# Kernel optimization log

Hardware: AMD Instinct MI355X
Metric: run time of the kernel (lower is better)

Reference implementation:

```python
import jax, jax.numpy as jnp
import numpy as np

EPS = 1e-6  # NAFNet LayerNorm2d eps
C = 64
B, H, W = 4, 128, 512


def _layer_norm_c(x, w, b):
    # x: [B,H,W,C]; normalize over channel dim (LayerNorm2d semantics)
    mu = jnp.mean(x, axis=-1, keepdims=True)
    var = jnp.mean(jnp.square(x - mu), axis=-1, keepdims=True)
    return (x - mu) * jax.lax.rsqrt(var + EPS) * w + b


def setup_inputs() -> dict:
    key = jax.random.key(0)
    ks = jax.random.split(key, 8)
    std = 1.0 / np.sqrt(C)  # conv1x1 fan-in init scale
    return {
        "x_l": jax.random.normal(ks[0], (B, C, H, W), jnp.float32),
        "x_r": jax.random.normal(ks[1], (B, C, H, W), jnp.float32),
        "norm_l_w": jnp.ones((C,), jnp.float32),
        "norm_l_b": jnp.zeros((C,), jnp.float32),
        "norm_r_w": jnp.ones((C,), jnp.float32),
        "norm_r_b": jnp.zeros((C,), jnp.float32),
        "l1_w": jax.random.normal(ks[2], (C, C), jnp.float32) * std,
        "l1_b": jnp.zeros((C,), jnp.float32),
        "r1_w": jax.random.normal(ks[3], (C, C), jnp.float32) * std,
        "r1_b": jnp.zeros((C,), jnp.float32),
        "l2_w": jax.random.normal(ks[4], (C, C), jnp.float32) * std,
        "l2_b": jnp.zeros((C,), jnp.float32),
        "r2_w": jax.random.normal(ks[5], (C, C), jnp.float32) * std,
        "r2_b": jnp.zeros((C,), jnp.float32),
        "beta": jax.random.normal(ks[6], (C,), jnp.float32) * 0.1,
        "gamma": jax.random.normal(ks[7], (C,), jnp.float32) * 0.1,
    }


def reference(x_l, x_r, norm_l_w, norm_l_b, norm_r_w, norm_r_b,
              l1_w, l1_b, r1_w, r1_b, l2_w, l2_b, r2_w, r2_b, beta, gamma):
    c = x_l.shape[1]
    scale = c ** (-0.5)
    # NCHW -> NHWC for channel-last math
    xl = jnp.transpose(x_l, (0, 2, 3, 1))  # [B,H,W,C]
    xr = jnp.transpose(x_r, (0, 2, 3, 1))

    # 1x1 conv == per-pixel linear: y = x @ W^T + b (W is [out,in])
    Q_l = jnp.einsum("bhwc,oc->bhwo", _layer_norm_c(xl, norm_l_w, norm_l_b), l1_w) + l1_b
    Q_r = jnp.einsum("bhwc,oc->bhwo", _layer_norm_c(xr, norm_r_w, norm_r_b), r1_w) + r1_b
    V_l = jnp.einsum("bhwc,oc->bhwo", xl, l2_w) + l2_b
    V_r = jnp.einsum("bhwc,oc->bhwo", xr, r2_w) + r2_b

    # row-wise cross-attention scores: [B,H,W_l,W_r]
    att = jnp.einsum("bhwc,bhvc->bhwv", Q_l, Q_r) * scale

    # right->left: softmax over W_r (last axis)
    F_r2l = jnp.einsum("bhwv,bhvc->bhwc", jax.nn.softmax(att, axis=-1), V_r)
    # left->right: softmax over W_l (axis -2 of att)
    F_l2r = jnp.einsum("bhwv,bhwc->bhvc", jax.nn.softmax(att, axis=-2), V_l)

    out_l = x_l + jnp.transpose(F_r2l * beta, (0, 3, 1, 2))
    out_r = x_r + jnp.transpose(F_l2r * gamma, (0, 3, 1, 2))
    return out_l, out_r
```

## Files before the change

### kernel.cpp

```cpp
#include <hip/hip_runtime.h>
#include <hip/hip_bf16.h>

#define HW_   65536
#define CHW_  4194304
#define OUTR_ 16777216
#define QSZ_  16777216

typedef __attribute__((ext_vector_type(4))) float    f32x4;
typedef __attribute__((ext_vector_type(8))) short    s16x8;
typedef __attribute__((ext_vector_type(4))) short    s16x4;
typedef __attribute__((ext_vector_type(4))) unsigned u32x4;
typedef __attribute__((ext_vector_type(2))) unsigned u32x2;

#define MFMA32(A,B,C) __builtin_amdgcn_mfma_f32_16x16x32_bf16((A),(B),(C),0,0,0)

#if __has_builtin(__builtin_amdgcn_mfma_f32_16x16x16bf16_1k)
#define MFMA16(A,B,C) __builtin_amdgcn_mfma_f32_16x16x16bf16_1k((A),(B),(C),0,0,0)
#else
__device__ __forceinline__ f32x4 mfma16_asm(s16x4 a, s16x4 b, f32x4 c){
  asm volatile("v_mfma_f32_16x16x16_bf16 %0, %1, %2, %0\n\ts_nop 7" : "+v"(c) : "v"(a), "v"(b));
  return c;
}
#define MFMA16(A,B,C) mfma16_asm((A),(B),(C))
#endif

#if __has_builtin(__builtin_amdgcn_exp2f)
#define EXP2(x) __builtin_amdgcn_exp2f(x)
#else
__device__ __forceinline__ float exp2_hw(float x){
  float r; asm("v_exp_f32 %0, %1\n\ts_nop 0" : "=v"(r) : "v"(x)); return r;
}
#define EXP2(x) exp2_hw(x)
#endif

#define QSCALE  0.18033688011112043f
#define SQSCALE 0.42466090350f

__device__ __forceinline__ unsigned short bf16u(float f) {
  union { __hip_bfloat16 h; unsigned short s; } x; x.h = __float2bfloat16(f); return x.s;
}
__device__ __forceinline__ unsigned pack2(float a, float b) {
  return (unsigned)bf16u(a) | ((unsigned)bf16u(b) << 16);
}
__device__ __forceinline__ float bflo(unsigned u) {
  union { unsigned q; float f; } x; x.q = u << 16; return x.f;
}
__device__ __forceinline__ float bfhi(unsigned u) {
  union { unsigned q; float f; } x; x.q = u & 0xFFFF0000u; return x.f;
}
__device__ __forceinline__ s16x8 as_s16x8(u32x4 u){ union{u32x4 a; s16x8 b;} x; x.a=u; return x.b; }
__device__ __forceinline__ s16x4 as_s16x4(u32x2 u){ union{u32x2 a; s16x4 b;} x; x.a=u; return x.b; }

__device__ __forceinline__ int swz128(int row, int bir) { return row*128 + (bir ^ ((row&7)<<4)); }
__device__ __forceinline__ int swzV(int c, int bir)    { return c*1024 + (bir ^ ((c&63)<<4)); }

__device__ __forceinline__ void ln32(const float* __restrict__ p, int base, int pix, int half,
                                     const float* __restrict__ w, const float* __restrict__ bb,
                                     char* buf, float* redS, float* redSS) {
  const int c0 = half*32;
  float xv[32], s = 0.f, ss = 0.f;
#pragma unroll
  for (int i = 0; i < 32; ++i) {
    float v = p[base + (c0+i)*HW_ + pix];
    xv[i] = v; s += v; ss = fmaf(v, v, ss);
  }
  redS[half*512 + pix] = s; redSS[half*512 + pix] = ss;
  __syncthreads();
  float st  = redS[pix]  + redS[512 + pix];
  float sst = redSS[pix] + redSS[512 + pix];
  float mu = st * 0.015625f;
  float rs = rsqrtf(fmaxf(sst * 0.015625f - mu*mu, 0.f) + 1e-6f);
#pragma unroll
  for (int i2 = 0; i2 < 4; ++i2) {
    u32x4 u;
#pragma unroll
    for (int e = 0; e < 4; ++e) {
      int i = i2*8 + e*2;
      float y0 = (xv[i  ]-mu)*rs*w[c0+i  ] + bb[c0+i  ];
      float y1 = (xv[i+1]-mu)*rs*w[c0+i+1] + bb[c0+i+1];
      u[e] = pack2(y0, y1);
    }
    *(u32x4*)(buf + swz128(pix, half*64 + i2*16)) = u;
  }
}

__device__ __forceinline__ void stageW(const float* __restrict__ Wg, char* bufW, int t) {
  int row = t >> 3, c0 = (t & 7) * 8;
  f32x4 f0 = *(const f32x4*)(Wg + row*64 + c0);
  f32x4 f1 = *(const f32x4*)(Wg + row*64 + c0 + 4);
  u32x4 u = { pack2(f0[0],f0[1]), pack2(f0[2],f0[3]), pack2(f1[0],f1[1]), pack2(f1[2],f1[3]) };
  *(u32x4*)(bufW + swz128(row, c0*2)) = u;
}

__device__ __forceinline__ void epi32(const char* bufG, const float* __restrict__ xres,
                                      const float* __restrict__ coef, float* __restrict__ outp,
                                      int base, int pix, int half) {
  const int c0 = half*32;
#pragma unroll
  for (int i2 = 0; i2 < 4; ++i2) {
    u32x4 gv = *(const u32x4*)(bufG + swz128(pix, half*64 + i2*16));
#pragma unroll
    for (int e = 0; e < 4; ++e) {
      int i = i2*8 + e*2;
      int idx = base + (c0+i)*HW_ + pix;
      outp[idx]       = xres[idx]       + coef[c0+i]   * bflo(gv[e]);
      outp[idx + HW_] = xres[idx + HW_] + coef[c0+i+1] * bfhi(gv[e]);
    }
  }
}

__global__ __launch_bounds__(1024)
void k1_prep(const float* __restrict__ xl, const float* __restrict__ xr,
             const float* __restrict__ nlw, const float* __restrict__ nlb,
             const float* __restrict__ nrw, const float* __restrict__ nrb,
             const float* __restrict__ l1w, const float* __restrict__ l1b,
             const float* __restrict__ r1w, const float* __restrict__ r1b,
             unsigned short* __restrict__ Qws) {
  __shared__ __align__(16) char bufA[65536];
  __shared__ __align__(16) char bufW[8192];
  __shared__ float redS[1024], redSS[1024];
  const int t = threadIdx.x, lane = t & 63, wave = t >> 6;
  const int pix = t & 511, half = t >> 9;
  const int g = lane >> 4, q15 = lane & 15;
  const int bh = blockIdx.x, b = bh >> 7, h = bh & 127;
  const int base = b*CHW_ + h*512;

#pragma unroll 1
  for (int s = 0; s < 2; ++s) {
    const float* x  = s ? xr  : xl;
    const float* w  = s ? nrw : nlw;
    const float* bb = s ? nrb : nlb;
    const float* W  = s ? r1w : l1w;
    const float* bi = s ? r1b : l1b;
    unsigned short* Qd = Qws + s*QSZ_ + bh*32768;
    if (s) __syncthreads();
    ln32(x, base, pix, half, w, bb, bufA, redS, redSS);
    if (t < 512) stageW(W, bufW, t);
    __syncthreads();
    {
      u32x4 a[2][2], wb[4][2];
#pragma unroll
      for (int mt = 0; mt < 2; ++mt)
#pragma unroll
        for (int hh = 0; hh < 2; ++hh)
          a[mt][hh] = *(const u32x4*)(bufA + swz128(wave*32 + mt*16 + q15, hh*64 + g*16));
#pragma unroll
      for (int ot = 0; ot < 4; ++ot)
#pragma unroll
        for (int hh = 0; hh < 2; ++hh)
          wb[ot][hh] = *(const u32x4*)(bufW + swz128(ot*16 + q15, hh*64 + g*16));
#pragma unroll
      for (int mt = 0; mt < 2; ++mt)
#pragma unroll
        for (int ot = 0; ot < 4; ++ot) {
          f32x4 z = {0.f,0.f,0.f,0.f};
          f32x4 acc = MFMA32(as_s16x8(a[mt][0]), as_s16x8(wb[ot][0]), z);
          acc = MFMA32(as_s16x8(a[mt][1]), as_s16x8(wb[ot][1]), acc);
          float bv = bi[ot*16 + q15];
#pragma unroll
          for (int rr = 0; rr < 4; ++rr)
            *(short*)(bufA + swz128(wave*32 + mt*16 + 4*g + rr, 2*(ot*16 + q15))) =
                (short)bf16u((acc[rr] + bv) * SQSCALE);
        }
    }
    __syncthreads();
#pragma unroll
    for (int i = 0; i < 4; ++i) {
      int seg = t*4 + i, row = seg >> 3, b16 = (seg & 7) * 16;
      u32x4 v = *(const u32x4*)(bufA + swz128(row, b16));
      *(u32x4*)((char*)Qd + row*128 + b16) = v;
    }
  }
}

__global__ __launch_bounds__(512)
void k2_fused(const unsigned short* __restrict__ Qws,
              const float* __restrict__ xl, const float* __restrict__ xr,
              const float* __restrict__ l2w, const float* __restrict__ l2b,
              const float* __restrict__ r2w, const float* __restrict__ r2b,
              const float* __restrict__ beta, const float* __restrict__ gamma,
              float* __restrict__ out) {
  __shared__ __align__(16) char ldsM[40960];
  __shared__ float lsumS[256];
  char* const Kc0 = ldsM;
  char* const Vc0 = ldsM + 16384;
  char* const bufW = ldsM + 32768;

  const int t = threadIdx.x, lane = t & 63, wave = t >> 6;
  const int g = lane >> 4, q15 = lane & 15;
  const int bid = blockIdx.x, qh = bid & 1, dir = (bid >> 1) & 1, bh = bid >> 2;
  const int b = bh >> 7, h = bh & 127;
  const int base = b*CHW_ + h*512;
  const char* Qb = (const char*)(Qws + dir*QSZ_ + bh*32768);
  const char* Kb = (const char*)(Qws + (1-dir)*QSZ_ + bh*32768);
  const float* xV   = dir ? xl : xr;
  const float* xres = dir ? xr : xl;
  const float* W2   = dir ? l2w : r2w;
  const float* b2   = dir ? l2b : r2b;
  const float* cf   = dir ? gamma : beta;
  float* outp = out + dir*OUTR_;

  const int qrow0 = qh*256 + wave*32;
  s16x8 qf[2][2];
#pragma unroll
  for (int qt = 0; qt < 2; ++qt)
#pragma unroll
    for (int hh = 0; hh < 2; ++hh)
      qf[qt][hh] = as_s16x8(*(const u32x4*)(Qb + (qrow0 + qt*16 + q15)*128 + hh*64 + g*16));

  stageW(W2, bufW, t);

  const int srow = t >> 3, sg = (t & 7) * 16, kv0 = (t & 7) * 8;
  {
    *(u32x4*)(Kc0 + swz128(srow, sg)) = *(const u32x4*)(Kb + srow*128 + sg);
    f32x4 f0 = *(const f32x4*)(xV + base + srow*HW_ + kv0);
    f32x4 f1 = *(const f32x4*)(xV + base + srow*HW_ + kv0 + 4);
    u32x4 vv = { pack2(f0[0],f0[1]), pack2(f0[2],f0[3]), pack2(f1[0],f1[1]), pack2(f1[2],f1[3]) };
    *(u32x4*)(Vc0 + swz128(srow, sg)) = vv;
  }
  __syncthreads();

  float lsum[2] = {0.f, 0.f};
  f32x4 O[2][4];
#pragma unroll
  for (int qt = 0; qt < 2; ++qt)
#pragma unroll
    for (int ct = 0; ct < 4; ++ct) { f32x4 z = {0.f,0.f,0.f,0.f}; O[qt][ct] = z; }

#pragma unroll 1
  for (int ch = 0; ch < 8; ++ch) {
    char* const Kc = Kc0 + (ch & 1)*8192;
    char* const Vc = Vc0 + (ch & 1)*8192;
    u32x4 kreg; f32x4 nf0, nf1;
    if (ch < 7) {
      kreg = *(const u32x4*)(Kb + ((ch+1)*64 + srow)*128 + sg);
      nf0  = *(const f32x4*)(xV + base + srow*HW_ + (ch+1)*64 + kv0);
      nf1  = *(const f32x4*)(xV + base + srow*HW_ + (ch+1)*64 + kv0 + 4);
    }
#pragma unroll
    for (int qt = 0; qt < 2; ++qt) {
      u32x2 pa[4];
      float sml = 0.f;
#pragma unroll
      for (int kb = 0; kb < 4; ++kb) {
        u32x4 k0 = *(const u32x4*)(Kc + swz128(kb*16 + q15, g*16));
        u32x4 k1 = *(const u32x4*)(Kc + swz128(kb*16 + q15, 64 + g*16));
        f32x4 z = {0.f,0.f,0.f,0.f};
        f32x4 s = MFMA32(as_s16x8(k0), qf[qt][0], z);
        s = MFMA32(as_s16x8(k1), qf[qt][1], s);
        float p0 = EXP2(s[0]), p1 = EXP2(s[1]), p2 = EXP2(s[2]), p3 = EXP2(s[3]);
        sml += (p0 + p1) + (p2 + p3);
        u32x2 pp = { pack2(p0, p1), pack2(p2, p3) };
        pa[kb] = pp;
      }
      lsum[qt] += sml;
#pragma unroll
      for (int ct = 0; ct < 4; ++ct) {
        int c = ct*16 + q15;
#pragma unroll
        for (int kb = 0; kb < 4; ++kb) {
          u32x2 vb = *(const u32x2*)(Vc + swz128(c, kb*32 + 8*g));
          O[qt][ct] = MFMA16(as_s16x4(pa[kb]), as_s16x4(vb), O[qt][ct]);
        }
      }
    }
    if (ch < 7) {
      char* const Kn = Kc0 + ((ch & 1)^1)*8192;
      char* const Vn = Vc0 + ((ch & 1)^1)*8192;
      *(u32x4*)(Kn + swz128(srow, sg)) = kreg;
      u32x4 vv = { pack2(nf0[0],nf0[1]), pack2(nf0[2],nf0[3]), pack2(nf1[0],nf1[1]), pack2(nf1[2],nf1[3]) };
      *(u32x4*)(Vn + swz128(srow, sg)) = vv;
    }
    __syncthreads();
  }

#pragma unroll
  for (int qt = 0; qt < 2; ++qt) {
    float l = lsum[qt];
    l += __shfl_xor(l, 16);
    l += __shfl_xor(l, 32);
    if (lane < 16) lsumS[wave*32 + qt*16 + q15] = l;
#pragma unroll
    for (int ct = 0; ct < 4; ++ct)
#pragma unroll
      for (int rr = 0; rr < 4; ++rr)
        *(short*)(ldsM + swz128(wave*32 + qt*16 + 4*g + rr, 2*(ct*16 + q15))) =
            (short)bf16u(O[qt][ct][rr]);
  }
  __syncthreads();

  {
    u32x4 a[2][2], wb[4][2];
#pragma unroll
    for (int mt = 0; mt < 2; ++mt)
#pragma unroll
      for (int hh = 0; hh < 2; ++hh)
        a[mt][hh] = *(const u32x4*)(ldsM + swz128(wave*32 + mt*16 + q15, hh*64 + g*16));
#pragma unroll
    for (int ot = 0; ot < 4; ++ot)
#pragma unroll
      for (int hh = 0; hh < 2; ++hh)
        wb[ot][hh] = *(const u32x4*)(bufW + swz128(ot*16 + q15, hh*64 + g*16));
#pragma unroll
    for (int mt = 0; mt < 2; ++mt)
#pragma unroll
      for (int ot = 0; ot < 4; ++ot) {
        f32x4 z = {0.f,0.f,0.f,0.f};
        f32x4 acc = MFMA32(as_s16x8(a[mt][0]), as_s16x8(wb[ot][0]), z);
        acc = MFMA32(as_s16x8(a[mt][1]), as_s16x8(wb[ot][1]), acc);
#pragma unroll
        for (int rr = 0; rr < 4; ++rr)
          *(short*)(ldsM + swz128(wave*32 + mt*16 + 4*g + rr, 2*(ot*16 + q15))) =
              (short)bf16u(acc[rr]);
      }
  }
  __syncthreads();

  {
    const int pl = t & 255, half2 = t >> 8;
    const int pix = qh*256 + pl;
    const float il = 1.f / lsumS[pl];
    const int c0 = half2*32;
#pragma unroll
    for (int i2 = 0; i2 < 4; ++i2) {
      u32x4 gv = *(const u32x4*)(ldsM + swz128(pl, half2*64 + i2*16));
#pragma unroll
      for (int e = 0; e < 4; ++e) {
        int c = c0 + i2*8 + e*2;
        int idx = base + c*HW_ + pix;
        outp[idx]       = xres[idx]       + cf[c]  *(bflo(gv[e])*il + b2[c]);
        outp[idx + HW_] = xres[idx + HW_] + cf[c+1]*(bfhi(gv[e])*il + b2[c+1]);
      }
    }
  }
}

__device__ __forceinline__ void stageV_m(const float* __restrict__ x, int base, char* bufV, int t) {
  int c = t >> 4, w0 = (t & 15) * 32;
#pragma unroll
  for (int i = 0; i < 4; ++i) {
    int w = w0 + i*8;
    f32x4 f0 = *(const f32x4*)(x + base + c*HW_ + w);
    f32x4 f1 = *(const f32x4*)(x + base + c*HW_ + w + 4);
    u32x4 u = { pack2(f0[0],f0[1]), pack2(f0[2],f0[3]), pack2(f1[0],f1[1]), pack2(f1[2],f1[3]) };
    *(u32x4*)(bufV + swzV(c, w*2)) = u;
  }
}
__device__ __forceinline__ void proj64_m(const char* bufIn, const char* bufW,
                                         const float* __restrict__ biasG,
                                         char* bufOut, int wave, int lane) {
  int g = lane >> 4, q15 = lane & 15;
  u32x4 a[2][2], wb[4][2];
#pragma unroll
  for (int mt = 0; mt < 2; ++mt)
#pragma unroll
    for (int h = 0; h < 2; ++h)
      a[mt][h] = *(const u32x4*)(bufIn + swz128(wave*32 + mt*16 + q15, h*64 + g*16));
#pragma unroll
  for (int ot = 0; ot < 4; ++ot)
#pragma unroll
    for (int h = 0; h < 2; ++h)
      wb[ot][h] = *(const u32x4*)(bufW + swz128(ot*16 + q15, h*64 + g*16));
#pragma unroll
  for (int mt = 0; mt < 2; ++mt)
#pragma unroll
    for (int ot = 0; ot < 4; ++ot) {
      f32x4 z = {0.f,0.f,0.f,0.f};
      f32x4 acc = MFMA32(as_s16x8(a[mt][0]), as_s16x8(wb[ot][0]), z);
      acc = MFMA32(as_s16x8(a[mt][1]), as_s16x8(wb[ot][1]), acc);
      float bv = biasG[ot*16 + q15];
#pragma unroll
      for (int rr = 0; rr < 4; ++rr)
        *(short*)(bufOut + swz128(wave*32 + mt*16 + 4*g + rr, 2*(ot*16 + q15))) =
            (short)bf16u(acc[rr] + bv);
    }
}
__device__ __forceinline__ void extract_q_m(const char* bufQ, int wave, int lane, s16x8 (&qf)[2][2]) {
  int g = lane >> 4, q15 = lane & 15;
#pragma unroll
  for (int qt = 0; qt < 2; ++qt)
#pragma unroll
    for (int h = 0; h < 2; ++h) {
      u32x4 u = *(const u32x4*)(bufQ + swz128(wave*32 + qt*16 + q15, h*64 + g*16));
#pragma unroll
      for (int e = 0; e < 4; ++e)
        u[e] = pack2(bflo(u[e])*QSCALE, bfhi(u[e])*QSCALE);
      qf[qt][h] = as_s16x8(u);
    }
}
__device__ __forceinline__ void flash_m(const char* bufK, const char* bufV, const s16x8 (&qf)[2][2],
                                        f32x4 (&O)[2][4], float (&lsum)[2], int lane) {
  int g = lane >> 4, q15 = lane & 15;
  float mref[2];
#pragma unroll
  for (int qt = 0; qt < 2; ++qt) {
    mref[qt] = -__builtin_inff(); lsum[qt] = 0.f;
#pragma unroll
    for (int ct = 0; ct < 4; ++ct) { f32x4 z = {0.f,0.f,0.f,0.f}; O[qt][ct] = z; }
  }
#pragma unroll 1
  for (int ch = 0; ch < 16; ++ch) {
    int kbase = ch * 32;
    u32x4 ka[2][2];
#pragma unroll
    for (int kb = 0; kb < 2; ++kb)
#pragma unroll
      for (int h = 0; h < 2; ++h)
        ka[kb][h] = *(const u32x4*)(bufK + swz128(kbase + kb*16 + q15, h*64 + g*16));
#pragma unroll
    for (int qt = 0; qt < 2; ++qt) {
      f32x4 z = {0.f,0.f,0.f,0.f};
      f32x4 a0 = MFMA32(as_s16x8(ka[0][0]), qf[qt][0], z);
      a0 = MFMA32(as_s16x8(ka[0][1]), qf[qt][1], a0);
      f32x4 a1 = MFMA32(as_s16x8(ka[1][0]), qf[qt][0], z);
      a1 = MFMA32(as_s16x8(ka[1][1]), qf[qt][1], a1);
      float cm = fmaxf(fmaxf(fmaxf(a0[0],a0[1]), fmaxf(a0[2],a0[3])),
                       fmaxf(fmaxf(a1[0],a1[1]), fmaxf(a1[2],a1[3])));
      cm = fmaxf(cm, __shfl_xor(cm, 16));
      cm = fmaxf(cm, __shfl_xor(cm, 32));
      if (__any(cm > mref[qt] + 8.f)) {
        float nm = fmaxf(mref[qt], cm);
        float corr = EXP2(mref[qt] - nm);
        lsum[qt] *= corr; mref[qt] = nm;
#pragma unroll
        for (int rr = 0; rr < 4; ++rr) {
          float cr = __shfl(corr, 4*g + rr);
#pragma unroll
          for (int ct = 0; ct < 4; ++ct) O[qt][ct][rr] *= cr;
        }
      }
      float p[8], sm = 0.f;
#pragma unroll
      for (int j = 0; j < 4; ++j) { p[j]   = EXP2(a0[j] - mref[qt]); sm += p[j]; }
#pragma unroll
      for (int j = 0; j < 4; ++j) { p[4+j] = EXP2(a1[j] - mref[qt]); sm += p[4+j]; }
      float s1 = sm + __shfl_xor(sm, 16);
      lsum[qt] += s1 + __shfl_xor(s1, 32);
      u32x2 pa0 = { pack2(p[0],p[1]), pack2(p[2],p[3]) };
      u32x2 pa1 = { pack2(p[4],p[5]), pack2(p[6],p[7]) };
#pragma unroll
      for (int ct = 0; ct < 4; ++ct) {
        int c = ct*16 + q15;
        u32x2 v0 = *(const u32x2*)(bufV + swzV(c, (kbase + 4*g)*2));
        u32x2 v1 = *(const u32x2*)(bufV + swzV(c, (kbase + 16 + 4*g)*2));
        O[qt][ct] = MFMA16(as_s16x4(pa0), as_s16x4(v0), O[qt][ct]);
        O[qt][ct] = MFMA16(as_s16x4(pa1), as_s16x4(v1), O[qt][ct]);
      }
    }
  }
}
__device__ __forceinline__ void write_O_m(char* buf, const f32x4 (&O)[2][4], const float (&lsum)[2],
                                          int wave, int lane) {
  int g = lane >> 4, q15 = lane & 15;
#pragma unroll
  for (int qt = 0; qt < 2; ++qt) {
    float inv = 1.f / lsum[qt];
    float invr[4];
#pragma unroll
    for (int rr = 0; rr < 4; ++rr) invr[rr] = __shfl(inv, 4*g + rr);
#pragma unroll
    for (int ct = 0; ct < 4; ++ct)
#pragma unroll
      for (int rr = 0; rr < 4; ++rr)
        *(short*)(buf + swz128(wave*32 + qt*16 + 4*g + rr, 2*(ct*16 + q15))) =
            (short)bf16u(O[qt][ct][rr] * invr[rr]);
  }
}
__device__ __forceinline__ void epi_ln_m(const char* bufG, const float* __restrict__ xres,
                                         const float* __restrict__ coef, float* __restrict__ outp,
                                         const float* __restrict__ w, const float* __restrict__ bb,
                                         char* bufLN, int base, int pix, int half,
                                         float* redS, float* redSS) {
  const int c0 = half*32;
  float xv[32], s = 0.f, ss = 0.f;
#pragma unroll
  for (int i2 = 0; i2 < 4; ++i2) {
    u32x4 gv = *(const u32x4*)(bufG + swz128(pix, half*64 + i2*16));
#pragma unroll
    for (int e = 0; e < 4; ++e) {
      int i = i2*8 + e*2;
      int idx = base + (c0+i)*HW_ + pix;
      float x0 = xres[idx], x1 = xres[idx + HW_];
      xv[i] = x0; xv[i+1] = x1;
      s += x0 + x1; ss = fmaf(x0,x0,ss); ss = fmaf(x1,x1,ss);
      outp[idx]       = x0 + coef[c0+i]   * bflo(gv[e]);
      outp[idx + HW_] = x1 + coef[c0+i+1] * bfhi(gv[e]);
    }
  }
  redS[half*512 + pix] = s; redSS[half*512 + pix] = ss;
  __syncthreads();
  float st  = redS[pix]  + redS[512 + pix];
  float sst = redSS[pix] + redSS[512 + pix];
  float mu = st * 0.015625f;
  float rs = rsqrtf(fmaxf(sst * 0.015625f - mu*mu, 0.f) + 1e-6f);
#pragma unroll
  for (int i2 = 0; i2 < 4; ++i2) {
    u32x4 u;
#pragma unroll
    for (int e = 0; e < 4; ++e) {
      int i = i2*8 + e*2;
      float y0 = (xv[i  ]-mu)*rs*w[c0+i  ] + bb[c0+i  ];
      float y1 = (xv[i+1]-mu)*rs*w[c0+i+1] + bb[c0+i+1];
      u[e] = pack2(y0, y1);
    }
    *(u32x4*)(bufLN + swz128(pix, half*64 + i2*16)) = u;
  }
}

__global__ __launch_bounds__(1024)
void scam_mono(const float* __restrict__ xl, const float* __restrict__ xr,
               const float* __restrict__ nlw, const float* __restrict__ nlb,
               const float* __restrict__ nrw, const float* __restrict__ nrb,
               const float* __restrict__ l1w, const float* __restrict__ l1b,
               const float* __restrict__ r1w, const float* __restrict__ r1b,
               const float* __restrict__ l2w, const float* __restrict__ l2b,
               const float* __restrict__ r2w, const float* __restrict__ r2b,
               const float* __restrict__ beta, const float* __restrict__ gamma,
               float* __restrict__ out) {
  __shared__ __align__(16) char bufA[65536];
  __shared__ __align__(16) char bufB[65536];
  __shared__ __align__(16) char bufW[8192];
  __shared__ float redS[1024];
  __shared__ float redSS[1024];
  const int t = threadIdx.x, lane = t & 63, wave = t >> 6;
  const int pix = t & 511, half = t >> 9;
  const int r = blockIdx.x, b = r >> 7, h = r & 127;
  const int base = b*CHW_ + h*512;

  if (t < 512) stageW(l1w, bufW, t);
  ln32(xl, base, pix, half, nlw, nlb, bufA, redS, redSS);
  __syncthreads();
  proj64_m(bufA, bufW, l1b, bufB, wave, lane);
  __syncthreads();
  s16x8 qfL[2][2];
  extract_q_m(bufB, wave, lane, qfL);
  if (t < 512) stageW(r1w, bufW, t);
  ln32(xr, base, pix, half, nrw, nrb, bufA, redS, redSS);
  __syncthreads();
  proj64_m(bufA, bufW, r1b, bufB, wave, lane);
  __syncthreads();
  stageV_m(xr, base, bufA, t);
  if (t < 512) stageW(r2w, bufW, t);
  __syncthreads();
  f32x4 O[2][4]; float lsum[2];
  flash_m(bufB, bufA, qfL, O, lsum, lane);
  s16x8 qfR[2][2];
  extract_q_m(bufB, wave, lane, qfR);
  __syncthreads();
  write_O_m(bufA, O, lsum, wave, lane);
  __syncthreads();
  proj64_m(bufA, bufW, r2b, bufB, wave, lane);
  __syncthreads();
  if (t < 512) stageW(l1w, bufW, t);
  epi_ln_m(bufB, xl, beta, out, nlw, nlb, bufA, base, pix, half, redS, redSS);
  __syncthreads();
  proj64_m(bufA, bufW, l1b, bufB, wave, lane);
  __syncthreads();
  stageV_m(xl, base, bufA, t);
  if (t < 512) stageW(l2w, bufW, t);
  __syncthreads();
  flash_m(bufB, bufA, qfR, O, lsum, lane);
  __syncthreads();
  write_O_m(bufA, O, lsum, wave, lane);
  __syncthreads();
  proj64_m(bufA, bufW, l2b, bufB, wave, lane);
  __syncthreads();
  epi32(bufB, xr, gamma, out + OUTR_, base, pix, half);
}

extern "C" void kernel_launch(void* const* d_in, const int* in_sizes, int n_in,
                              void* d_out, int out_size, void* d_ws, size_t ws_size,
                              hipStream_t stream) {
  (void)in_sizes; (void)n_in; (void)out_size;
  const float* xl  = (const float*)d_in[0];
  const float* xr  = (const float*)d_in[1];
  const float* nlw = (const float*)d_in[2];
  const float* nlb = (const float*)d_in[3];
  const float* nrw = (const float*)d_in[4];
  const float* nrb = (const float*)d_in[5];
  const float* l1w = (const float*)d_in[6];
  const float* l1b = (const float*)d_in[7];
  const float* r1w = (const float*)d_in[8];
  const float* r1b = (const float*)d_in[9];
  const float* l2w = (const float*)d_in[10];
  const float* l2b = (const float*)d_in[11];
  const float* r2w = (const float*)d_in[12];
  const float* r2b = (const float*)d_in[13];
  const float* beta  = (const float*)d_in[14];
  const float* gamma = (const float*)d_in[15];
  float* out = (float*)d_out;

  if (ws_size >= (size_t)2 * QSZ_ * sizeof(unsigned short)) {
    unsigned short* Qws = (unsigned short*)d_ws;
    k1_prep<<<dim3(512), dim3(1024), 0, stream>>>(
        xl, xr, nlw, nlb, nrw, nrb, l1w, l1b, r1w, r1b, Qws);
    k2_fused<<<dim3(2048), dim3(512), 0, stream>>>(
        Qws, xl, xr, l2w, l2b, r2w, r2b, beta, gamma, out);
  } else {
    scam_mono<<<dim3(512), dim3(1024), 0, stream>>>(
        xl, xr, nlw, nlb, nrw, nrb, l1w, l1b, r1w, r1b,
        l2w, l2b, r2w, r2b, beta, gamma, out);
  }
}
```

Before: 190.0 us.

## Compute softmax row sums via MFMA with ones, remap block order

```diff
diff --git a/kernel.cpp b/kernel.cpp
--- a/kernel.cpp
+++ b/kernel.cpp
@@ -181,14 +181,16 @@
               const float* __restrict__ beta, const float* __restrict__ gamma,
               float* __restrict__ out) {
   __shared__ __align__(16) char ldsM[40960];
-  __shared__ float lsumS[256];
   char* const Kc0 = ldsM;
   char* const Vc0 = ldsM + 16384;
   char* const bufW = ldsM + 32768;
 
   const int t = threadIdx.x, lane = t & 63, wave = t >> 6;
   const int g = lane >> 4, q15 = lane & 15;
-  const int bid = blockIdx.x, qh = bid & 1, dir = (bid >> 1) & 1, bh = bid >> 2;
+  const int bid = blockIdx.x;
+  const int xg = bid & 7, j = bid >> 3;
+  const int bh = xg + 8*(j >> 2);
+  const int sub = j & 3, dir = sub >> 1, qh = sub & 1;
   const int b = bh >> 7, h = bh & 127;
   const int base = b*CHW_ + h*512;
   const char* Qb = (const char*)(Qws + dir*QSZ_ + bh*32768);
@@ -220,12 +222,16 @@
   }
   __syncthreads();
 
-  float lsum[2] = {0.f, 0.f};
+  const s16x4 ones = { (short)0x3F80, (short)0x3F80, (short)0x3F80, (short)0x3F80 };
+  f32x4 S_acc[2];
   f32x4 O[2][4];
 #pragma unroll
-  for (int qt = 0; qt < 2; ++qt)
-#pragma unroll
-    for (int ct = 0; ct < 4; ++ct) { f32x4 z = {0.f,0.f,0.f,0.f}; O[qt][ct] = z; }
+  for (int qt = 0; qt < 2; ++qt) {
+    f32x4 z = {0.f,0.f,0.f,0.f};
+    S_acc[qt] = z;
+#pragma unroll
+    for (int ct = 0; ct < 4; ++ct) O[qt][ct] = z;
+  }
 
 #pragma unroll 1
   for (int ch = 0; ch < 8; ++ch) {
@@ -240,7 +246,6 @@
 #pragma unroll
     for (int qt = 0; qt < 2; ++qt) {
       u32x2 pa[4];
-      float sml = 0.f;
 #pragma unroll
       for (int kb = 0; kb < 4; ++kb) {
         u32x4 k0 = *(const u32x4*)(Kc + swz128(kb*16 + q15, g*16));
@@ -248,12 +253,12 @@
         f32x4 z = {0.f,0.f,0.f,0.f};
         f32x4 s = MFMA32(as_s16x8(k0), qf[qt][0], z);
         s = MFMA32(as_s16x8(k1), qf[qt][1], s);
-        float p0 = EXP2(s[0]), p1 = EXP2(s[1]), p2 = EXP2(s[2]), p3 = EXP2(s[3]);
-        sml += (p0 + p1) + (p2 + p3);
-        u32x2 pp = { pack2(p0, p1), pack2(p2, p3) };
+        u32x2 pp = { pack2(EXP2(s[0]), EXP2(s[1])), pack2(EXP2(s[2]), EXP2(s[3])) };
         pa[kb] = pp;
       }
-      lsum[qt] += sml;
+#pragma unroll
+      for (int kb = 0; kb < 4; ++kb)
+        S_acc[qt] = MFMA16(as_s16x4(pa[kb]), ones, S_acc[qt]);
 #pragma unroll
       for (int ct = 0; ct < 4; ++ct) {
         int c = ct*16 + q15;
@@ -276,16 +281,15 @@
 
 #pragma unroll
   for (int qt = 0; qt < 2; ++qt) {
-    float l = lsum[qt];
-    l += __shfl_xor(l, 16);
-    l += __shfl_xor(l, 32);
-    if (lane < 16) lsumS[wave*32 + qt*16 + q15] = l;
+    f32x4 inv;
+#pragma unroll
+    for (int rr = 0; rr < 4; ++rr) inv[rr] = 1.f / S_acc[qt][rr];
 #pragma unroll
     for (int ct = 0; ct < 4; ++ct)
 #pragma unroll
       for (int rr = 0; rr < 4; ++rr)
         *(short*)(ldsM + swz128(wave*32 + qt*16 + 4*g + rr, 2*(ct*16 + q15))) =
-            (short)bf16u(O[qt][ct][rr]);
+            (short)bf16u(O[qt][ct][rr] * inv[rr]);
   }
   __syncthreads();
 
@@ -308,10 +312,11 @@
         f32x4 z = {0.f,0.f,0.f,0.f};
         f32x4 acc = MFMA32(as_s16x8(a[mt][0]), as_s16x8(wb[ot][0]), z);
         acc = MFMA32(as_s16x8(a[mt][1]), as_s16x8(wb[ot][1]), acc);
+        float bv = b2[ot*16 + q15];
 #pragma unroll
         for (int rr = 0; rr < 4; ++rr)
           *(short*)(ldsM + swz128(wave*32 + mt*16 + 4*g + rr, 2*(ot*16 + q15))) =
-              (short)bf16u(acc[rr]);
+              (short)bf16u(acc[rr] + bv);
       }
   }
   __syncthreads();
@@ -319,7 +324,6 @@
   {
     const int pl = t & 255, half2 = t >> 8;
     const int pix = qh*256 + pl;
-    const float il = 1.f / lsumS[pl];
     const int c0 = half2*32;
 #pragma unroll
     for (int i2 = 0; i2 < 4; ++i2) {
@@ -328,8 +332,8 @@
       for (int e = 0; e < 4; ++e) {
         int c = c0 + i2*8 + e*2;
         int idx = base + c*HW_ + pix;
-        outp[idx]       = xres[idx]       + cf[c]  *(bflo(gv[e])*il + b2[c]);
-        outp[idx + HW_] = xres[idx + HW_] + cf[c+1]*(bfhi(gv[e])*il + b2[c+1]);
+        outp[idx]       = xres[idx]       + cf[c]  *bflo(gv[e]);
+        outp[idx + HW_] = xres[idx + HW_] + cf[c+1]*bfhi(gv[e]);
       }
     }
   }
```

Result: faster. 182.9 us (-3.7%).
